# Kernel tuning notes

Hardware: AMD Instinct MI355X
Metric: run time of the kernel (lower is better)

The kernel has to match this reference:

```python
import jax, jax.numpy as jnp
import numpy as np

N_NODES = 50000
N_EDGES = 800000
D_IN = 64   # input_dimension + 1
D_HID = 64


def _gcn_conv(x, src, dst, W, b, deg_isqrt):
    # PyG GCNConv: X' = D^{-1/2} (A + I) D^{-1/2} X W + b
    h = x @ W  # [N, H]
    norm = (deg_isqrt[src] * deg_isqrt[dst])[:, None]  # [E, 1]
    agg = jax.ops.segment_sum(h[src] * norm, dst, num_segments=x.shape[0])
    # self-loop contribution: norm_ii = deg_isqrt[i]^2
    agg = agg + h * (deg_isqrt * deg_isqrt)[:, None]
    return agg + b


def setup_inputs() -> dict:
    key = jax.random.key(0)
    ks = jax.random.split(key, 8)
    x = jax.random.normal(ks[0], (N_NODES, D_IN), dtype=jnp.float32)
    edge_index = jax.random.randint(ks[1], (2, N_EDGES), 0, N_NODES, dtype=jnp.int32)
    s = 1.0 / np.sqrt(D_HID)
    W0 = jax.random.normal(ks[2], (D_IN, D_HID), dtype=jnp.float32) * s
    b0 = jnp.zeros((D_HID,), dtype=jnp.float32)
    W1 = jax.random.normal(ks[3], (D_HID, D_HID), dtype=jnp.float32) * s
    b1 = jnp.zeros((D_HID,), dtype=jnp.float32)
    W2 = jax.random.normal(ks[4], (D_HID, D_HID), dtype=jnp.float32) * s
    b2 = jnp.zeros((D_HID,), dtype=jnp.float32)
    Wout = jax.random.normal(ks[5], (D_HID, 1), dtype=jnp.float32) * s
    bout = jnp.zeros((1,), dtype=jnp.float32)
    return {"x": x, "edge_index": edge_index, "W0": W0, "b0": b0,
            "W1": W1, "b1": b1, "W2": W2, "b2": b2,
            "Wout": Wout, "bout": bout}


def reference(x, edge_index, W0, b0, W1, b1, W2, b2, Wout, bout):
    src, dst = edge_index[0], edge_index[1]
    n = x.shape[0]
    # degree with self-loop (edge weight 1.0 each)
    deg = jnp.zeros((n,), x.dtype).at[dst].add(1.0) + 1.0
    deg_isqrt = jax.lax.rsqrt(deg)
    h = jax.nn.relu(_gcn_conv(x, src, dst, W0, b0, deg_isqrt))
    h = jax.nn.relu(_gcn_conv(h, src, dst, W1, b1, deg_isqrt))
    h = jax.nn.relu(_gcn_conv(h, src, dst, W2, b2, deg_isqrt))
    return h @ Wout + bout  # [N, 1]
```

## Files before the change

### kernel.cpp

```cpp
#include <hip/hip_runtime.h>
#include <hip/hip_bf16.h>

#define D 64
#define N_NODES 50000
#define N_EDGES 800000
#define TILE 16

__global__ void scan1_k(const int* __restrict__ cnt, int* __restrict__ off,
                        int* __restrict__ bsum, float* __restrict__ dis, int N) {
    __shared__ int sh[256];
    int t = threadIdx.x;
    int i = blockIdx.x * 256 + t;
    int v = (i < N) ? cnt[i] : 0;
    sh[t] = v;
    __syncthreads();
#pragma unroll
    for (int d = 1; d < 256; d <<= 1) {
        int u = (t >= d) ? sh[t - d] : 0;
        __syncthreads();
        sh[t] += u;
        __syncthreads();
    }
    if (i < N) {
        off[i] = sh[t] - v;
        dis[i] = rsqrtf((float)v + 1.0f);
    }
    if (t == 255) bsum[blockIdx.x] = sh[255];
}

__global__ void scan2_k(int* __restrict__ bsum, int nb) {
    __shared__ int sh[256];
    int t = threadIdx.x;
    int v = (t < nb) ? bsum[t] : 0;
    sh[t] = v;
    __syncthreads();
#pragma unroll
    for (int d = 1; d < 256; d <<= 1) {
        int u = (t >= d) ? sh[t - d] : 0;
        __syncthreads();
        sh[t] += u;
        __syncthreads();
    }
    if (t < nb) bsum[t] = sh[t] - v;
}

__global__ void scan3_k(int* __restrict__ off, const int* __restrict__ bsum,
                        int* __restrict__ cursor, int N, int E) {
    int i = blockIdx.x * 256 + threadIdx.x;
    if (i < N) {
        int o = off[i] + bsum[blockIdx.x];
        off[i] = o;
        cursor[i] = o;
    }
    if (i == 0) off[N] = E;
}

__device__ __forceinline__ void fma4(float4& a, float s, float4 w) {
    a.x = fmaf(s, w.x, a.x);
    a.y = fmaf(s, w.y, a.y);
    a.z = fmaf(s, w.z, a.z);
    a.w = fmaf(s, w.w, a.w);
}

template <int SCALED>
__device__ __forceinline__ void tile_gemm(const float (*hbuf)[68], const float4* __restrict__ W4,
                                          const float* __restrict__ dis, float* __restrict__ outp,
                                          int base, int t) {
    int lane = t & 63;
    int cg = lane & 15;
    int rr = (t >> 6) * 4 + (lane >> 4);
    float4 acc = make_float4(0.f, 0.f, 0.f, 0.f);
#pragma unroll
    for (int kk = 0; kk < 16; ++kk) {
        float4 hb = *(const float4*)&hbuf[rr][kk * 4];
        fma4(acc, hb.x, W4[(kk * 4 + 0) * 16 + cg]);
        fma4(acc, hb.y, W4[(kk * 4 + 1) * 16 + cg]);
        fma4(acc, hb.z, W4[(kk * 4 + 2) * 16 + cg]);
        fma4(acc, hb.w, W4[(kk * 4 + 3) * 16 + cg]);
    }
    if (SCALED) {
        float dv = dis[base + rr];
        acc.x *= dv; acc.y *= dv; acc.z *= dv; acc.w *= dv;
    }
    ((float4*)outp)[(size_t)(base + rr) * 16 + cg] = acc;
}

__global__ void fused_pre_k(const float4* __restrict__ X4, const float4* __restrict__ W4,
                            float* __restrict__ H, const int* __restrict__ dst,
                            int* __restrict__ cnt, int N, int E, int gemmBlocks) {
    __shared__ float hbuf[TILE][68];
    int bid = blockIdx.x;
    int t = threadIdx.x;
    if (bid < gemmBlocks) {
        int base = bid * TILE;
        int r = t >> 4, ch = t & 15;
        float4 v = X4[(size_t)(base + r) * 16 + ch];
        *(float4*)&hbuf[r][ch * 4] = v;
        __syncthreads();
        tile_gemm<0>(hbuf, W4, nullptr, H, base, t);
    } else {
        int hb = bid - gemmBlocks;
        int nhb = gridDim.x - gemmBlocks;
        for (int i = hb * 256 + t; i < E; i += nhb * 256) {
            atomicAdd(&cnt[dst[i]], 1);
        }
    }
}

__global__ void fused_fill_k(const int* __restrict__ src, const int* __restrict__ dst,
                             int* __restrict__ cursor, int* __restrict__ esrc,
                             float4* __restrict__ H4, const float* __restrict__ dis,
                             int N, int E, int fillBlocks) {
    int bid = blockIdx.x;
    int t = threadIdx.x;
    if (bid < fillBlocks) {
        for (int i = bid * 256 + t; i < E; i += fillBlocks * 256) {
            int pos = atomicAdd(&cursor[dst[i]], 1);
            esrc[pos] = src[i];
        }
    } else {
        int sb = bid - fillBlocks;
        int nsb = gridDim.x - fillBlocks;
        int total = N * 16;
        for (int i = sb * 256 + t; i < total; i += nsb * 256) {
            float4 v = H4[i];
            float dv = dis[i >> 4];
            v.x *= dv; v.y *= dv; v.z *= dv; v.w *= dv;
            H4[i] = v;
        }
    }
}

template <int FINAL>
__global__ void layer_k(const float4* __restrict__ Hs4, const int* __restrict__ off,
                        const int* __restrict__ esrc, const float* __restrict__ dis,
                        const float* __restrict__ bias, const float4* __restrict__ W4,
                        const float* __restrict__ bout, float* __restrict__ outp, int N) {
    __shared__ float hbuf[TILE][68];
    int t = threadIdx.x;
    int lane = t & 63;
    int w = t >> 6;
    int g = lane >> 4;
    int l16 = lane & 15;
    int rloc = w * 4 + g;
    int n = blockIdx.x * TILE + rloc;

    int beg = off[n], end = off[n + 1];
    float4 acc = Hs4[(size_t)n * 16 + l16];
    int j = beg;
    for (; j + 7 < end; j += 8) {
        int s0 = esrc[j],     s1 = esrc[j + 1], s2 = esrc[j + 2], s3 = esrc[j + 3];
        int s4 = esrc[j + 4], s5 = esrc[j + 5], s6 = esrc[j + 6], s7 = esrc[j + 7];
        float4 v0 = Hs4[(size_t)s0 * 16 + l16];
        float4 v1 = Hs4[(size_t)s1 * 16 + l16];
        float4 v2 = Hs4[(size_t)s2 * 16 + l16];
        float4 v3 = Hs4[(size_t)s3 * 16 + l16];
        float4 v4 = Hs4[(size_t)s4 * 16 + l16];
        float4 v5 = Hs4[(size_t)s5 * 16 + l16];
        float4 v6 = Hs4[(size_t)s6 * 16 + l16];
        float4 v7 = Hs4[(size_t)s7 * 16 + l16];
        acc.x += ((v0.x + v1.x) + (v2.x + v3.x)) + ((v4.x + v5.x) + (v6.x + v7.x));
        acc.y += ((v0.y + v1.y) + (v2.y + v3.y)) + ((v4.y + v5.y) + (v6.y + v7.y));
        acc.z += ((v0.z + v1.z) + (v2.z + v3.z)) + ((v4.z + v5.z) + (v6.z + v7.z));
        acc.w += ((v0.w + v1.w) + (v2.w + v3.w)) + ((v4.w + v5.w) + (v6.w + v7.w));
    }
    for (; j < end; ++j) {
        float4 v = Hs4[(size_t)esrc[j] * 16 + l16];
        acc.x += v.x; acc.y += v.y; acc.z += v.z; acc.w += v.w;
    }

    float dv = dis[n];
    float4 b4 = ((const float4*)bias)[l16];
    float4 h4;
    h4.x = fmaxf(fmaf(acc.x, dv, b4.x), 0.f);
    h4.y = fmaxf(fmaf(acc.y, dv, b4.y), 0.f);
    h4.z = fmaxf(fmaf(acc.z, dv, b4.z), 0.f);
    h4.w = fmaxf(fmaf(acc.w, dv, b4.w), 0.f);

    if (FINAL) {
        float4 w4 = ((const float4*)W4)[l16];
        float p = fmaf(h4.x, w4.x, fmaf(h4.y, w4.y, fmaf(h4.z, w4.z, h4.w * w4.w)));
        p += __shfl_xor(p, 1, 64);
        p += __shfl_xor(p, 2, 64);
        p += __shfl_xor(p, 4, 64);
        p += __shfl_xor(p, 8, 64);
        if (l16 == 0) outp[n] = p + bout[0];
    } else {
        *(float4*)&hbuf[rloc][l16 * 4] = h4;
        __syncthreads();
        tile_gemm<1>(hbuf, W4, dis, outp, blockIdx.x * TILE, t);
    }
}

extern "C" void kernel_launch(void* const* d_in, const int* in_sizes, int n_in,
                              void* d_out, int out_size, void* d_ws, size_t ws_size,
                              hipStream_t stream) {
    const float* x    = (const float*)d_in[0];
    const int*   ei   = (const int*)d_in[1];
    const float* W0   = (const float*)d_in[2];
    const float* b0   = (const float*)d_in[3];
    const float* W1   = (const float*)d_in[4];
    const float* b1   = (const float*)d_in[5];
    const float* W2   = (const float*)d_in[6];
    const float* b2   = (const float*)d_in[7];
    const float* Wout = (const float*)d_in[8];
    const float* bout = (const float*)d_in[9];
    float* out = (float*)d_out;

    const int N = N_NODES, E = N_EDGES;
    const int* src = ei;
    const int* dst = ei + E;

    char* ws = (char*)d_ws;
    int*   cnt    = (int*)(ws);
    int*   off    = (int*)(ws + (256u << 10));
    int*   cursor = (int*)(ws + (512u << 10));
    float* dis    = (float*)(ws + (768u << 10));
    int*   bsum   = (int*)(ws + (990u << 10));
    int*   esrc   = (int*)(ws + (1u << 20));
    float* bufA   = (float*)(ws + (5u << 20));
    float* bufB   = (float*)(ws + (18u << 20));

    dim3 blk(256);
    const int NB = (N + 255) / 256;
    dim3 gN(NB);
    const int TILES = N / TILE;
    dim3 gTile(TILES);
    const int HIST_BLOCKS = 1563;
    const int FILL_BLOCKS = 3125;
    const int SCALE_BLOCKS = 784;

    hipMemsetAsync(cnt, 0, (size_t)N * sizeof(int), stream);
    fused_pre_k<<<dim3(TILES + HIST_BLOCKS), blk, 0, stream>>>(
        (const float4*)x, (const float4*)W0, bufA, dst, cnt, N, E, TILES);

    scan1_k<<<gN, blk, 0, stream>>>(cnt, off, bsum, dis, N);
    scan2_k<<<1, blk, 0, stream>>>(bsum, NB);
    scan3_k<<<gN, blk, 0, stream>>>(off, bsum, cursor, N, E);

    fused_fill_k<<<dim3(FILL_BLOCKS + SCALE_BLOCKS), blk, 0, stream>>>(
        src, dst, cursor, esrc, (float4*)bufA, dis, N, E, FILL_BLOCKS);

    layer_k<0><<<gTile, blk, 0, stream>>>((const float4*)bufA, off, esrc, dis,
                                          b0, (const float4*)W1, nullptr, bufB, N);
    layer_k<0><<<gTile, blk, 0, stream>>>((const float4*)bufB, off, esrc, dis,
                                          b1, (const float4*)W2, nullptr, bufA, N);
    layer_k<1><<<gTile, blk, 0, stream>>>((const float4*)bufA, off, esrc, dis,
                                          b2, (const float4*)Wout, bout, out, N);
}
```

Measured before the change: 314.6 us.

## Split fused hist/GEMM kernel and batch gather tail with masked loads

Splits the fused first-layer GEMM plus degree-histogram kernel into two separate launches: a one-edge-per-thread histogram kernel and a standalone tile GEMM kernel. In the aggregation kernel, the scalar remainder loop after the 8-way unrolled gather becomes a single 8-wide batch with clamped indices and zero masks, so all remainder loads are issued together. This trades one extra launch and some redundant loads of a repeated index for more memory-level parallelism and less divergence in the tail. The unrolled loop's bound check is rewritten in an equivalent form.

```diff
diff --git a/kernel.cpp b/kernel.cpp
--- a/kernel.cpp
+++ b/kernel.cpp
@@ -5,6 +5,11 @@
 #define N_NODES 50000
 #define N_EDGES 800000
 #define TILE 16
+
+__global__ void hist_k(const int* __restrict__ dst, int* __restrict__ cnt, int E) {
+    int i = blockIdx.x * blockDim.x + threadIdx.x;
+    if (i < E) atomicAdd(&cnt[dst[i]], 1);
+}
 
 __global__ void scan1_k(const int* __restrict__ cnt, int* __restrict__ off,
                         int* __restrict__ bsum, float* __restrict__ dis, int N) {
@@ -85,26 +90,16 @@
     ((float4*)outp)[(size_t)(base + rr) * 16 + cg] = acc;
 }
 
-__global__ void fused_pre_k(const float4* __restrict__ X4, const float4* __restrict__ W4,
-                            float* __restrict__ H, const int* __restrict__ dst,
-                            int* __restrict__ cnt, int N, int E, int gemmBlocks) {
+__global__ void gemm0_k(const float4* __restrict__ X4, const float4* __restrict__ W4,
+                        float* __restrict__ H, int N) {
     __shared__ float hbuf[TILE][68];
-    int bid = blockIdx.x;
-    int t = threadIdx.x;
-    if (bid < gemmBlocks) {
-        int base = bid * TILE;
-        int r = t >> 4, ch = t & 15;
-        float4 v = X4[(size_t)(base + r) * 16 + ch];
-        *(float4*)&hbuf[r][ch * 4] = v;
-        __syncthreads();
-        tile_gemm<0>(hbuf, W4, nullptr, H, base, t);
-    } else {
-        int hb = bid - gemmBlocks;
-        int nhb = gridDim.x - gemmBlocks;
-        for (int i = hb * 256 + t; i < E; i += nhb * 256) {
-            atomicAdd(&cnt[dst[i]], 1);
-        }
-    }
+    int t = threadIdx.x;
+    int base = blockIdx.x * TILE;
+    int r = t >> 4, ch = t & 15;
+    float4 v = X4[(size_t)(base + r) * 16 + ch];
+    *(float4*)&hbuf[r][ch * 4] = v;
+    __syncthreads();
+    tile_gemm<0>(hbuf, W4, nullptr, H, base, t);
 }
 
 __global__ void fused_fill_k(const int* __restrict__ src, const int* __restrict__ dst,
@@ -148,7 +143,7 @@
     int beg = off[n], end = off[n + 1];
     float4 acc = Hs4[(size_t)n * 16 + l16];
     int j = beg;
-    for (; j + 7 < end; j += 8) {
+    for (; j + 8 <= end; j += 8) {
         int s0 = esrc[j],     s1 = esrc[j + 1], s2 = esrc[j + 2], s3 = esrc[j + 3];
         int s4 = esrc[j + 4], s5 = esrc[j + 5], s6 = esrc[j + 6], s7 = esrc[j + 7];
         float4 v0 = Hs4[(size_t)s0 * 16 + l16];
@@ -164,9 +159,40 @@
         acc.z += ((v0.z + v1.z) + (v2.z + v3.z)) + ((v4.z + v5.z) + (v6.z + v7.z));
         acc.w += ((v0.w + v1.w) + (v2.w + v3.w)) + ((v4.w + v5.w) + (v6.w + v7.w));
     }
-    for (; j < end; ++j) {
-        float4 v = Hs4[(size_t)esrc[j] * 16 + l16];
-        acc.x += v.x; acc.y += v.y; acc.z += v.z; acc.w += v.w;
+    if (j < end) {
+        int last = end - 1;
+        int i1 = j + 1 <= last ? j + 1 : last;
+        int i2 = j + 2 <= last ? j + 2 : last;
+        int i3 = j + 3 <= last ? j + 3 : last;
+        int i4 = j + 4 <= last ? j + 4 : last;
+        int i5 = j + 5 <= last ? j + 5 : last;
+        int i6 = j + 6 <= last ? j + 6 : last;
+        int i7 = j + 7 <= last ? j + 7 : last;
+        int s0 = esrc[j],  s1 = esrc[i1], s2 = esrc[i2], s3 = esrc[i3];
+        int s4 = esrc[i4], s5 = esrc[i5], s6 = esrc[i6], s7 = esrc[i7];
+        float m1 = (j + 1 < end) ? 1.f : 0.f;
+        float m2 = (j + 2 < end) ? 1.f : 0.f;
+        float m3 = (j + 3 < end) ? 1.f : 0.f;
+        float m4 = (j + 4 < end) ? 1.f : 0.f;
+        float m5 = (j + 5 < end) ? 1.f : 0.f;
+        float m6 = (j + 6 < end) ? 1.f : 0.f;
+        float m7 = (j + 7 < end) ? 1.f : 0.f;
+        float4 v0 = Hs4[(size_t)s0 * 16 + l16];
+        float4 v1 = Hs4[(size_t)s1 * 16 + l16];
+        float4 v2 = Hs4[(size_t)s2 * 16 + l16];
+        float4 v3 = Hs4[(size_t)s3 * 16 + l16];
+        float4 v4 = Hs4[(size_t)s4 * 16 + l16];
+        float4 v5 = Hs4[(size_t)s5 * 16 + l16];
+        float4 v6 = Hs4[(size_t)s6 * 16 + l16];
+        float4 v7 = Hs4[(size_t)s7 * 16 + l16];
+        acc.x += v0.x;           acc.y += v0.y;           acc.z += v0.z;           acc.w += v0.w;
+        acc.x = fmaf(m1, v1.x, acc.x); acc.y = fmaf(m1, v1.y, acc.y); acc.z = fmaf(m1, v1.z, acc.z); acc.w = fmaf(m1, v1.w, acc.w);
+        acc.x = fmaf(m2, v2.x, acc.x); acc.y = fmaf(m2, v2.y, acc.y); acc.z = fmaf(m2, v2.z, acc.z); acc.w = fmaf(m2, v2.w, acc.w);
+        acc.x = fmaf(m3, v3.x, acc.x); acc.y = fmaf(m3, v3.y, acc.y); acc.z = fmaf(m3, v3.z, acc.z); acc.w = fmaf(m3, v3.w, acc.w);
+        acc.x = fmaf(m4, v4.x, acc.x); acc.y = fmaf(m4, v4.y, acc.y); acc.z = fmaf(m4, v4.z, acc.z); acc.w = fmaf(m4, v4.w, acc.w);
+        acc.x = fmaf(m5, v5.x, acc.x); acc.y = fmaf(m5, v5.y, acc.y); acc.z = fmaf(m5, v5.z, acc.z); acc.w = fmaf(m5, v5.w, acc.w);
+        acc.x = fmaf(m6, v6.x, acc.x); acc.y = fmaf(m6, v6.y, acc.y); acc.z = fmaf(m6, v6.z, acc.z); acc.w = fmaf(m6, v6.w, acc.w);
+        acc.x = fmaf(m7, v7.x, acc.x); acc.y = fmaf(m7, v7.y, acc.y); acc.z = fmaf(m7, v7.z, acc.z); acc.w = fmaf(m7, v7.w, acc.w);
     }
 
     float dv = dis[n];
@@ -224,15 +250,15 @@
     dim3 blk(256);
     const int NB = (N + 255) / 256;
     dim3 gN(NB);
+    dim3 gE((E + 255) / 256);
     const int TILES = N / TILE;
     dim3 gTile(TILES);
-    const int HIST_BLOCKS = 1563;
     const int FILL_BLOCKS = 3125;
     const int SCALE_BLOCKS = 784;
 
     hipMemsetAsync(cnt, 0, (size_t)N * sizeof(int), stream);
-    fused_pre_k<<<dim3(TILES + HIST_BLOCKS), blk, 0, stream>>>(
-        (const float4*)x, (const float4*)W0, bufA, dst, cnt, N, E, TILES);
+    hist_k<<<gE, blk, 0, stream>>>(dst, cnt, E);
+    gemm0_k<<<gTile, blk, 0, stream>>>((const float4*)x, (const float4*)W0, bufA, N);
 
     scan1_k<<<gN, blk, 0, stream>>>(cnt, off, bsum, dis, N);
     scan2_k<<<1, blk, 0, stream>>>(bsum, NB);
```

New measurement: 307.4 us. 2.3% less time.
